# Kernel optimization log

Hardware: AMD Instinct MI355X
Metric: run time of the kernel (lower is better)

The kernel has to match this reference:

```python
import jax, jax.numpy as jnp
import numpy as np

B, T, D = 8, 2048, 1024
H, C, DV = 8, 64, 128   # n_heads, latent_dim, d_head
LN_EPS = 1e-5
NORM_EPS = 1e-12  # F.normalize eps


def _xavier(k, shape, fan_in, fan_out):
    lim = float(np.sqrt(6.0 / (fan_in + fan_out)))
    return jax.random.uniform(k, shape, jnp.float32, -lim, lim)


def setup_inputs() -> dict:
    key = jax.random.key(0)
    ks = jax.random.split(key, 9)
    x = jax.random.normal(ks[0], (B, T, D), jnp.float32)
    Wq = _xavier(ks[1], (C, D), D, C)            # S_q weight (out,in)
    Wk = _xavier(ks[2], (C, D), D, C)            # S_k
    Wv = _xavier(ks[3], (C, D), D, C)            # S_v
    Qc = _xavier(ks[4], (H, C, C), C, C)         # per-head latent rotations
    Vc = _xavier(ks[5], (H, C, DV), C, DV)       # per-head value up-proj
    Wa_w = _xavier(ks[6], (H * C, D), D, H * C)  # W_alpha weight
    Wa_b = jnp.full((H * C,), 3.0, jnp.float32)  # W_alpha bias init = 3.0
    Wo = _xavier(ks[7], (D, H * DV), H * DV, D)  # output proj
    gamma = jnp.ones((D,), jnp.float32)
    beta = jnp.zeros((D,), jnp.float32)
    return {"x": x, "Wq": Wq, "Wk": Wk, "Wv": Wv, "Qc": Qc, "Vc": Vc,
            "Wa_w": Wa_w, "Wa_b": Wa_b, "Wo": Wo, "gamma": gamma, "beta": beta}


def _forward(x, Wq, Wk, Wv, Qc, Vc, Wa_w, Wa_b, Wo, gamma, beta):
    residual = x
    # LayerNorm (biased variance, like torch)
    mu = jnp.mean(x, axis=-1, keepdims=True)
    var = jnp.mean(jnp.square(x - mu), axis=-1, keepdims=True)
    xn = (x - mu) * jax.lax.rsqrt(var + LN_EPS) * gamma + beta

    q_lat = xn @ Wq.T          # (B,T,C)
    k_lat = xn @ Wk.T          # (B,T,C) shared across heads
    v_lat = xn @ Wv.T          # (B,T,C)

    q = jnp.einsum('btc,hce->bhte', q_lat, Qc)   # (B,H,T,C)
    v = jnp.einsum('btc,hcd->bhtd', v_lat, Vc)   # (B,H,T,DV)
    alpha = jax.nn.sigmoid(xn @ Wa_w.T + Wa_b)   # (B,T,H*C)
    alpha = alpha.reshape(x.shape[0], x.shape[1], H, C).transpose(0, 2, 1, 3)  # (B,H,T,C)

    # F.normalize(k, dim=-1): k / max(||k||, eps)
    kn = k_lat / jnp.maximum(jnp.linalg.norm(k_lat, axis=-1, keepdims=True), NORM_EPS)

    # time-major for scan
    qs = jnp.moveaxis(q, 2, 0)      # (T,B,H,C)
    vs = jnp.moveaxis(v, 2, 0)      # (T,B,H,DV)
    als = jnp.moveaxis(alpha, 2, 0)  # (T,B,H,C)
    kns = jnp.moveaxis(kn, 1, 0)    # (T,B,C)

    S0 = jnp.zeros((x.shape[0], H, C, DV), x.dtype)

    def step(S, inp):
        q_t, k_t, v_t, a_t = inp
        # S_t = diag(alpha_t) S_{t-1} + k_t v_t^T  (k shared across heads)
        S = a_t[..., None] * S + k_t[:, None, :, None] * v_t[..., None, :]
        o_t = jnp.einsum('bhcv,bhc->bhv', S, q_t)
        return S, o_t

    _, outs = jax.lax.scan(step, S0, (qs, kns, vs, als))  # outs: (T,B,H,DV)
    out = jnp.moveaxis(outs, 0, 1).reshape(x.shape[0], x.shape[1], H * DV)
    return out @ Wo.T + residual


def reference(x, Wq, Wk, Wv, Qc, Vc, Wa_w, Wa_b, Wo, gamma, beta):
    return _forward(x, Wq, Wk, Wv, Qc, Vc, Wa_w, Wa_b, Wo, gamma, beta)
```

## Files before the change

kernel.cpp:

```cpp
#include <hip/hip_runtime.h>

typedef unsigned short u16;
typedef unsigned int   u32;
typedef __bf16 bf16x8 __attribute__((ext_vector_type(8)));
typedef float  f32x4  __attribute__((ext_vector_type(4)));

#define B_  8
#define T_  2048
#define D_  1024
#define H_  8
#define C_  64
#define DV_ 128
#define M_  (B_*T_)
#define L_  128
#define NC_ (T_/L_)
#define TS_ 8

__device__ __forceinline__ u16 f2bf(float f){
  u32 u = __float_as_uint(f);
  u32 r = (u + 0x7fffu + ((u >> 16) & 1u)) >> 16;
  return (u16)r;
}
__device__ __forceinline__ float bf2f(u16 u){
  return __uint_as_float(((u32)u) << 16);
}

__global__ __launch_bounds__(256) void ln_kernel(
    const float* __restrict__ x, const float* __restrict__ gamma,
    const float* __restrict__ beta, u16* __restrict__ xnb){
  const int m = blockIdx.x;
  const int tid = threadIdx.x;
  const int wave = tid >> 6, lane = tid & 63;
  const float* xr = x + (size_t)m * D_;
  float4 xv = *(const float4*)&xr[tid*4];
  float s = xv.x + xv.y + xv.z + xv.w;
  #pragma unroll
  for (int off = 32; off > 0; off >>= 1) s += __shfl_xor(s, off, 64);
  __shared__ float red[8];
  if (lane == 0) red[wave] = s;
  __syncthreads();
  float mu = (red[0]+red[1]+red[2]+red[3]) * (1.f/1024.f);
  float dx = xv.x-mu, dy = xv.y-mu, dz = xv.z-mu, dw = xv.w-mu;
  float ss = dx*dx + dy*dy + dz*dz + dw*dw;
  #pragma unroll
  for (int off = 32; off > 0; off >>= 1) ss += __shfl_xor(ss, off, 64);
  if (lane == 0) red[4+wave] = ss;
  __syncthreads();
  float var = (red[4]+red[5]+red[6]+red[7]) * (1.f/1024.f);
  float rs = rsqrtf(var + 1e-5f);
  float4 g  = *(const float4*)&gamma[tid*4];
  float4 bb = *(const float4*)&beta[tid*4];
  ushort4 o4;
  o4.x = f2bf(dx*rs*g.x + bb.x);
  o4.y = f2bf(dy*rs*g.y + bb.y);
  o4.z = f2bf(dz*rs*g.z + bb.z);
  o4.w = f2bf(dw*rs*g.w + bb.w);
  *(ushort4*)&xnb[(size_t)m*D_ + tid*4] = o4;
}

__global__ __launch_bounds__(256) void prep_weights(
    const float* __restrict__ Wq, const float* __restrict__ Wk,
    const float* __restrict__ Wv, const float* __restrict__ Wa,
    const float* __restrict__ Qc, const float* __restrict__ Vc,
    const float* __restrict__ Wo,
    u16* __restrict__ Wcatb, u16* __restrict__ QcTb,
    u16* __restrict__ VcTb,  u16* __restrict__ Wob){
  int idx = blockIdx.x * 256 + threadIdx.x;
  if (idx < 720896){
    int r = idx >> 10, col = idx & 1023;
    float v;
    if (r < 64)       v = Wq[(size_t)r*1024 + col];
    else if (r < 128) v = Wk[(size_t)(r-64)*1024 + col];
    else if (r < 192) v = Wv[(size_t)(r-128)*1024 + col];
    else              v = Wa[(size_t)(r-192)*1024 + col];
    Wcatb[idx] = f2bf(v);
  } else if (idx < 753664){
    int i = idx - 720896;
    int n = i >> 6, c = i & 63; int h = n >> 6, e = n & 63;
    QcTb[i] = f2bf(Qc[((size_t)h*64 + c)*64 + e]);
  } else if (idx < 819200){
    int i = idx - 753664;
    int n = i >> 6, c = i & 63; int h = n >> 7, d = n & 127;
    VcTb[i] = f2bf(Vc[((size_t)h*64 + c)*128 + d]);
  } else if (idx < 1867776){
    int i = idx - 819200;
    Wob[i] = f2bf(Wo[i]);
  }
}

__global__ __launch_bounds__(256) void gemm_bf16(
    const u16* __restrict__ A, const u16* __restrict__ Bw,
    float* __restrict__ C, const float* __restrict__ res,
    u16* __restrict__ Cb, int N, int K){
  __shared__ u16 As[128][36];
  __shared__ u16 Bs[64][36];
  const int tid = threadIdx.x;
  const int wave = tid >> 6;
  const int lane = tid & 63;
  const int q  = lane >> 4;
  const int mr = lane & 15;
  const int m0 = blockIdx.x * 128;
  const int n0 = blockIdx.y * 64;

  union FragU { u32 u[4]; bf16x8 v; };
  f32x4 zero = {0.f, 0.f, 0.f, 0.f};
  f32x4 acc[2][4];
  #pragma unroll
  for (int i = 0; i < 2; i++)
    #pragma unroll
    for (int j = 0; j < 4; j++) acc[i][j] = zero;

  for (int k0 = 0; k0 < K; k0 += 32){
    #pragma unroll
    for (int p = 0; p < 2; ++p){
      int ch = p*256 + tid;
      int r = ch >> 2, c4 = ch & 3;
      const uint4 val = *(const uint4*)(&A[(size_t)(m0 + r)*K + k0 + c4*8]);
      u32* dst = (u32*)&As[r][c4*8];
      dst[0]=val.x; dst[1]=val.y; dst[2]=val.z; dst[3]=val.w;
    }
    {
      int r = tid >> 2, c4 = tid & 3;
      const uint4 val = *(const uint4*)(&Bw[(size_t)(n0 + r)*K + k0 + c4*8]);
      u32* dst = (u32*)&Bs[r][c4*8];
      dst[0]=val.x; dst[1]=val.y; dst[2]=val.z; dst[3]=val.w;
    }
    __syncthreads();
    bf16x8 afr[2], bfr[4];
    #pragma unroll
    for (int mt = 0; mt < 2; mt++){
      const u32* p = (const u32*)&As[wave*32 + mt*16 + mr][q*8];
      FragU f; f.u[0]=p[0]; f.u[1]=p[1]; f.u[2]=p[2]; f.u[3]=p[3];
      afr[mt] = f.v;
    }
    #pragma unroll
    for (int nt = 0; nt < 4; nt++){
      const u32* p = (const u32*)&Bs[nt*16 + mr][q*8];
      FragU f; f.u[0]=p[0]; f.u[1]=p[1]; f.u[2]=p[2]; f.u[3]=p[3];
      bfr[nt] = f.v;
    }
    #pragma unroll
    for (int mt = 0; mt < 2; mt++)
      #pragma unroll
      for (int nt = 0; nt < 4; nt++)
        acc[mt][nt] = __builtin_amdgcn_mfma_f32_16x16x32_bf16(
            afr[mt], bfr[nt], acc[mt][nt], 0, 0, 0);
    __syncthreads();
  }

  #pragma unroll
  for (int mt = 0; mt < 2; mt++)
    #pragma unroll
    for (int nt = 0; nt < 4; nt++)
      #pragma unroll
      for (int r = 0; r < 4; r++){
        int row = m0 + wave*32 + mt*16 + q*4 + r;
        int col = n0 + nt*16 + mr;
        size_t idx = (size_t)row * N + col;
        float v = acc[mt][nt][r];
        if (res) v += res[idx];
        if (Cb) Cb[idx] = f2bf(v);
        else    C[idx] = v;
      }
}

__global__ __launch_bounds__(256) void split_proj(
    const float* __restrict__ proj, const float* __restrict__ Wab,
    u16* __restrict__ qlatb, float* __restrict__ knf,
    u16* __restrict__ vlatb, float* __restrict__ alphaf){
  const int m = blockIdx.x * 4 + (threadIdx.x >> 6);
  const int lane = threadIdx.x & 63;
  const float* pr = proj + (size_t)m * 704;
  qlatb[(size_t)m*64 + lane] = f2bf(pr[lane]);
  float kv = pr[64 + lane];
  float ss = kv * kv;
  #pragma unroll
  for (int off = 32; off > 0; off >>= 1) ss += __shfl_xor(ss, off, 64);
  float nrm = fmaxf(sqrtf(ss), 1e-12f);
  knf[(size_t)m*64 + lane] = kv / nrm;
  vlatb[(size_t)m*64 + lane] = f2bf(pr[128 + lane]);
  #pragma unroll
  for (int j = 0; j < 8; j++){
    int jj = j*64 + lane;
    float av = pr[192 + jj] + Wab[jj];
    alphaf[(size_t)m*512 + jj] = 1.f / (1.f + expf(-av));
  }
}


__global__ __launch_bounds__(512, 2) void scan_pass1(
    const float* __restrict__ knf, const u16* __restrict__ vb,
    const float* __restrict__ alphaf,
    float* __restrict__ Sbuf, float* __restrict__ btot){
  const int ch = blockIdx.x;
  const int bh = blockIdx.y;
  const int b = bh >> 3, h = bh & 7;
  const int tid = threadIdx.x;
  const int g = tid >> 7;
  const int d = tid & 127;
  const int t0 = ch * L_;
  __shared__ __align__(16) float sK[TS_][64];
  __shared__ __align__(16) float sA[TS_][64];
  __shared__ __align__(16) float sV[TS_][128];

  const float* kbase = knf    + ((size_t)(b*T_ + t0))*64;
  const float* abase = alphaf + ((size_t)(b*T_ + t0))*512 + h*64;
  const u16*   vbase = vb     + ((size_t)(b*T_ + t0))*1024 + h*128;

  float S[16];
  #pragma unroll
  for (int i = 0; i < 16; i++) S[i] = 0.f;
  float bt = 1.f;

  const int ts = tid >> 6, cs = tid & 63;
  for (int sb = 0; sb < L_/TS_; sb++){
    const int tb = sb * TS_;
    sK[ts][cs] = kbase[(size_t)(tb+ts)*64 + cs];
    sA[ts][cs] = abase[(size_t)(tb+ts)*512 + cs];
    {
      int i1 = 512 + tid;
      sV[tid>>7][tid&127] = bf2f(vbase[(size_t)(tb+(tid>>7))*1024 + (tid&127)]);
      sV[i1 >>7][i1 &127] = bf2f(vbase[(size_t)(tb+(i1 >>7))*1024 + (i1 &127)]);
    }
    __syncthreads();
    #pragma unroll 1
    for (int tt = 0; tt < TS_; tt++){
      const float vd = sV[tt][d];
      #pragma unroll
      for (int i4 = 0; i4 < 4; i4++){
        float4 a4 = *(const float4*)&sA[tt][g*16 + i4*4];
        float4 k4 = *(const float4*)&sK[tt][g*16 + i4*4];
        S[i4*4+0] = a4.x*S[i4*4+0] + k4.x*vd;
        S[i4*4+1] = a4.y*S[i4*4+1] + k4.y*vd;
        S[i4*4+2] = a4.z*S[i4*4+2] + k4.z*vd;
        S[i4*4+3] = a4.w*S[i4*4+3] + k4.w*vd;
      }
      if (d < 16) bt *= sA[tt][g*16 + d];
      __builtin_amdgcn_sched_barrier(0);
    }
    __syncthreads();
  }
  float* Sl = Sbuf + ((size_t)bh*NC_ + ch) * (64*128);
  #pragma unroll
  for (int i = 0; i < 16; i++) Sl[(size_t)(g*16+i)*128 + d] = S[i];
  if (d < 16) btot[((size_t)bh*NC_ + ch)*64 + g*16 + d] = bt;
}

__global__ __launch_bounds__(256) void scan_combine(
    float* __restrict__ Sbuf, const float* __restrict__ btot){
  const int bh = blockIdx.x;
  const int tid = threadIdx.x;
  float S[32];
  #pragma unroll
  for (int i = 0; i < 32; i++) S[i] = 0.f;
  float*       Sb  = Sbuf + (size_t)bh*NC_*8192;
  const float* btb = btot + (size_t)bh*NC_*64;
  for (int j = 0; j < NC_; j++){
    if (j < NC_-1){
      #pragma unroll
      for (int i = 0; i < 32; i++){
        int e = i*256 + tid;
        float loc = Sb[(size_t)j*8192 + e];
        float bv  = btb[j*64 + (e >> 7)];
        Sb[(size_t)j*8192 + e] = S[i];
        S[i] = bv * S[i] + loc;
      }
    } else {
      #pragma unroll
      for (int i = 0; i < 32; i++) Sb[(size_t)j*8192 + i*256 + tid] = S[i];
    }
  }
}

__global__ __launch_bounds__(512, 2) void scan_pass2(
    const float* __restrict__ qf, const float* __restrict__ knf,
    const u16* __restrict__ vb, const float* __restrict__ alphaf,
    const float* __restrict__ Sbuf, u16* __restrict__ ob){
  const int ch = blockIdx.x;
  const int bh = blockIdx.y;
  const int b = bh >> 3, h = bh & 7;
  const int tid = threadIdx.x;
  const int g = tid >> 7;
  const int d = tid & 127;
  const int t0 = ch * L_;
  __shared__ __align__(16) float sQ[TS_][64];
  __shared__ __align__(16) float sK[TS_][64];
  __shared__ __align__(16) float sA[TS_][64];
  __shared__ __align__(16) float sV[TS_][128];
  __shared__ __align__(16) float sO[4][TS_][128];

  const float* qbase = qf     + ((size_t)(b*T_ + t0))*512 + h*64;
  const float* kbase = knf    + ((size_t)(b*T_ + t0))*64;
  const float* abase = alphaf + ((size_t)(b*T_ + t0))*512 + h*64;
  const u16*   vbase = vb     + ((size_t)(b*T_ + t0))*1024 + h*128;
  u16*         obase = ob     + ((size_t)(b*T_ + t0))*1024 + h*128;

  float S[16];
  const float* Si = Sbuf + ((size_t)bh*NC_ + ch) * (64*128);
  #pragma unroll
  for (int i = 0; i < 16; i++) S[i] = Si[(size_t)(g*16+i)*128 + d];

  const int ts = tid >> 6, cs = tid & 63;
  for (int sb = 0; sb < L_/TS_; sb++){
    const int tb = sb * TS_;
    sQ[ts][cs] = qbase[(size_t)(tb+ts)*512 + cs];
    sK[ts][cs] = kbase[(size_t)(tb+ts)*64 + cs];
    sA[ts][cs] = abase[(size_t)(tb+ts)*512 + cs];
    {
      int i1 = 512 + tid;
      sV[tid>>7][tid&127] = bf2f(vbase[(size_t)(tb+(tid>>7))*1024 + (tid&127)]);
      sV[i1 >>7][i1 &127] = bf2f(vbase[(size_t)(tb+(i1 >>7))*1024 + (i1 &127)]);
    }
    __syncthreads();
    #pragma unroll 1
    for (int tt = 0; tt < TS_; tt++){
      const float vd = sV[tt][d];
      float o = 0.f;
      #pragma unroll
      for (int i4 = 0; i4 < 4; i4++){
        float4 a4 = *(const float4*)&sA[tt][g*16 + i4*4];
        float4 k4 = *(const float4*)&sK[tt][g*16 + i4*4];
        float4 q4 = *(const float4*)&sQ[tt][g*16 + i4*4];
        S[i4*4+0] = a4.x*S[i4*4+0] + k4.x*vd;  o += S[i4*4+0]*q4.x;
        S[i4*4+1] = a4.y*S[i4*4+1] + k4.y*vd;  o += S[i4*4+1]*q4.y;
        S[i4*4+2] = a4.z*S[i4*4+2] + k4.z*vd;  o += S[i4*4+2]*q4.z;
        S[i4*4+3] = a4.w*S[i4*4+3] + k4.w*vd;  o += S[i4*4+3]*q4.w;
      }
      sO[g][tt][d] = o;
      __builtin_amdgcn_sched_barrier(0);
    }
    __syncthreads();
    #pragma unroll
    for (int i = 0; i < 2; i++){
      int idx = i*512 + tid;
      int tt = idx >> 7, dd = idx & 127;
      float o = sO[0][tt][dd] + sO[1][tt][dd] + sO[2][tt][dd] + sO[3][tt][dd];
      obase[(size_t)(tb+tt)*1024 + dd] = f2bf(o);
    }
  }
}

extern "C" void kernel_launch(void* const* d_in, const int* in_sizes, int n_in,
                              void* d_out, int out_size, void* d_ws, size_t ws_size,
                              hipStream_t stream){
  const float* x     = (const float*)d_in[0];
  const float* Wq    = (const float*)d_in[1];
  const float* Wk    = (const float*)d_in[2];
  const float* Wv    = (const float*)d_in[3];
  const float* Qc    = (const float*)d_in[4];
  const float* Vc    = (const float*)d_in[5];
  const float* Wa_w  = (const float*)d_in[6];
  const float* Wa_b  = (const float*)d_in[7];
  const float* Wo    = (const float*)d_in[8];
  const float* gamma = (const float*)d_in[9];
  const float* beta  = (const float*)d_in[10];
  float* out = (float*)d_out;

  char* ws = (char*)d_ws;
  size_t off = 0;
  auto alloc = [&](size_t bytes) -> void* {
    void* p = ws + off; off += (bytes + 255) & ~(size_t)255; return p;
  };
  char* R1 = (char*)alloc((size_t)M_ * 1024 * 2);
  u16*   xnb  = (u16*)R1;
  u16*   obuf = (u16*)R1;
  char* R2 = (char*)alloc((size_t)M_ * 704 * 4);
  float* proj = (float*)R2;
  float* qf   = (float*)R2;
  float* Sbuf   = (float*)alloc((size_t)64 * NC_ * 8192 * 4);
  u16*   vfb    = (u16*)alloc((size_t)M_ * 1024 * 2);
  float* alphaf = (float*)alloc((size_t)M_ * 512 * 4);
  float* knf    = (float*)alloc((size_t)M_ * 64 * 4);
  u16*   qlatb  = (u16*)alloc((size_t)M_ * 64 * 2);
  u16*   vlatb  = (u16*)alloc((size_t)M_ * 64 * 2);
  u16*   Wcatb  = (u16*)alloc((size_t)704 * 1024 * 2);
  u16*   QcTb   = (u16*)alloc((size_t)512 * 64 * 2);
  u16*   VcTb   = (u16*)alloc((size_t)1024 * 64 * 2);
  u16*   Wob    = (u16*)alloc((size_t)1024 * 1024 * 2);
  float* btotp  = (float*)alloc((size_t)64 * NC_ * 64 * 4);
  (void)ws_size; (void)in_sizes; (void)n_in; (void)out_size;

  ln_kernel<<<dim3(M_), dim3(256), 0, stream>>>(x, gamma, beta, xnb);
  prep_weights<<<dim3(7296), dim3(256), 0, stream>>>(
      Wq, Wk, Wv, Wa_w, Qc, Vc, Wo, Wcatb, QcTb, VcTb, Wob);
  gemm_bf16<<<dim3(M_/128, 704/64), dim3(256), 0, stream>>>(
      xnb, Wcatb, proj, nullptr, nullptr, 704, 1024);
  split_proj<<<dim3(M_/4), dim3(256), 0, stream>>>(
      proj, Wa_b, qlatb, knf, vlatb, alphaf);
  gemm_bf16<<<dim3(M_/128, 1024/64), dim3(256), 0, stream>>>(
      vlatb, VcTb, nullptr, nullptr, vfb, 1024, 64);
  gemm_bf16<<<dim3(M_/128, 512/64), dim3(256), 0, stream>>>(
      qlatb, QcTb, qf, nullptr, nullptr, 512, 64);
  scan_pass1<<<dim3(NC_-1, 64), dim3(512), 0, stream>>>(
      knf, vfb, alphaf, Sbuf, btotp);
  scan_combine<<<dim3(64), dim3(256), 0, stream>>>(Sbuf, btotp);
  scan_pass2<<<dim3(NC_, 64), dim3(512), 0, stream>>>(
      qf, knf, vfb, alphaf, Sbuf, obuf);
  gemm_bf16<<<dim3(M_/128, 1024/64), dim3(256), 0, stream>>>(
      obuf, Wob, out, x, nullptr, 1024, 1024);
}
```

Before: 567.7 us.

## Load scan k/alpha/q via scalar loads instead of LDS staging in scan passes

Both scan kernels stop staging k, alpha, q and v through shared memory with block barriers. Each wave now reads its 16-element alpha/k/q slices straight into scalar registers with inline s_load_dwordx16, and reads v directly from global memory. Launch bounds are raised so more blocks can be resident per CU. This targets LDS traffic and barrier stalls, but each timestep now waits on a scalar-load round trip. The added barrier in pass2 guards reuse of the sO buffer across sub-blocks.

```diff
diff --git a/kernel.cpp b/kernel.cpp
--- a/kernel.cpp
+++ b/kernel.cpp
@@ -4,6 +4,7 @@
 typedef unsigned int   u32;
 typedef __bf16 bf16x8 __attribute__((ext_vector_type(8)));
 typedef float  f32x4  __attribute__((ext_vector_type(4)));
+typedef float  f32x16 __attribute__((ext_vector_type(16)));
 
 #define B_  8
 #define T_  2048
@@ -188,7 +189,26 @@
 }
 
 
-__global__ __launch_bounds__(512, 2) void scan_pass1(
+__device__ __forceinline__ void sload2(const float* ap, const float* kp,
+                                       f32x16& a16, f32x16& k16){
+  asm volatile("s_load_dwordx16 %0, %2, 0x0\n\t"
+               "s_load_dwordx16 %1, %3, 0x0\n\t"
+               "s_waitcnt lgkmcnt(0)"
+               : "=&s"(a16), "=&s"(k16)
+               : "s"(ap), "s"(kp));
+}
+__device__ __forceinline__ void sload3(const float* ap, const float* kp,
+                                       const float* qp,
+                                       f32x16& a16, f32x16& k16, f32x16& q16){
+  asm volatile("s_load_dwordx16 %0, %3, 0x0\n\t"
+               "s_load_dwordx16 %1, %4, 0x0\n\t"
+               "s_load_dwordx16 %2, %5, 0x0\n\t"
+               "s_waitcnt lgkmcnt(0)"
+               : "=&s"(a16), "=&s"(k16), "=&s"(q16)
+               : "s"(ap), "s"(kp), "s"(qp));
+}
+
+__global__ __launch_bounds__(512, 8) void scan_pass1(
     const float* __restrict__ knf, const u16* __restrict__ vb,
     const float* __restrict__ alphaf,
     float* __restrict__ Sbuf, float* __restrict__ btot){
@@ -196,50 +216,32 @@
   const int bh = blockIdx.y;
   const int b = bh >> 3, h = bh & 7;
   const int tid = threadIdx.x;
-  const int g = tid >> 7;
+  const int g = __builtin_amdgcn_readfirstlane(tid >> 7);
   const int d = tid & 127;
   const int t0 = ch * L_;
-  __shared__ __align__(16) float sK[TS_][64];
-  __shared__ __align__(16) float sA[TS_][64];
-  __shared__ __align__(16) float sV[TS_][128];
-
-  const float* kbase = knf    + ((size_t)(b*T_ + t0))*64;
-  const float* abase = alphaf + ((size_t)(b*T_ + t0))*512 + h*64;
-  const u16*   vbase = vb     + ((size_t)(b*T_ + t0))*1024 + h*128;
+
+  const float* kp = knf    + ((size_t)(b*T_ + t0))*64  + g*16;
+  const float* ap = alphaf + ((size_t)(b*T_ + t0))*512 + h*64 + g*16;
+  const u16*   vp = vb     + ((size_t)(b*T_ + t0))*1024 + h*128 + d;
 
   float S[16];
   #pragma unroll
   for (int i = 0; i < 16; i++) S[i] = 0.f;
   float bt = 1.f;
 
-  const int ts = tid >> 6, cs = tid & 63;
-  for (int sb = 0; sb < L_/TS_; sb++){
-    const int tb = sb * TS_;
-    sK[ts][cs] = kbase[(size_t)(tb+ts)*64 + cs];
-    sA[ts][cs] = abase[(size_t)(tb+ts)*512 + cs];
-    {
-      int i1 = 512 + tid;
-      sV[tid>>7][tid&127] = bf2f(vbase[(size_t)(tb+(tid>>7))*1024 + (tid&127)]);
-      sV[i1 >>7][i1 &127] = bf2f(vbase[(size_t)(tb+(i1 >>7))*1024 + (i1 &127)]);
-    }
-    __syncthreads();
-    #pragma unroll 1
-    for (int tt = 0; tt < TS_; tt++){
-      const float vd = sV[tt][d];
-      #pragma unroll
-      for (int i4 = 0; i4 < 4; i4++){
-        float4 a4 = *(const float4*)&sA[tt][g*16 + i4*4];
-        float4 k4 = *(const float4*)&sK[tt][g*16 + i4*4];
-        S[i4*4+0] = a4.x*S[i4*4+0] + k4.x*vd;
-        S[i4*4+1] = a4.y*S[i4*4+1] + k4.y*vd;
-        S[i4*4+2] = a4.z*S[i4*4+2] + k4.z*vd;
-        S[i4*4+3] = a4.w*S[i4*4+3] + k4.w*vd;
-      }
-      if (d < 16) bt *= sA[tt][g*16 + d];
-      __builtin_amdgcn_sched_barrier(0);
-    }
-    __syncthreads();
-  }
+  for (int t = 0; t < L_; t++){
+    float vd = bf2f(vp[0]);
+    float al = 1.f;
+    if (d < 16) al = ap[d];
+    f32x16 a16, k16;
+    sload2(ap, kp, a16, k16);
+    #pragma unroll
+    for (int i = 0; i < 16; i++)
+      S[i] = a16[i]*S[i] + k16[i]*vd;
+    bt *= al;
+    kp += 64; ap += 512; vp += 1024;
+  }
+
   float* Sl = Sbuf + ((size_t)bh*NC_ + ch) * (64*128);
   #pragma unroll
   for (int i = 0; i < 16; i++) Sl[(size_t)(g*16+i)*128 + d] = S[i];
@@ -272,7 +274,7 @@
   }
 }
 
-__global__ __launch_bounds__(512, 2) void scan_pass2(
+__global__ __launch_bounds__(512, 8) void scan_pass2(
     const float* __restrict__ qf, const float* __restrict__ knf,
     const u16* __restrict__ vb, const float* __restrict__ alphaf,
     const float* __restrict__ Sbuf, u16* __restrict__ ob){
@@ -280,54 +282,38 @@
   const int bh = blockIdx.y;
   const int b = bh >> 3, h = bh & 7;
   const int tid = threadIdx.x;
-  const int g = tid >> 7;
+  const int g = __builtin_amdgcn_readfirstlane(tid >> 7);
   const int d = tid & 127;
   const int t0 = ch * L_;
-  __shared__ __align__(16) float sQ[TS_][64];
-  __shared__ __align__(16) float sK[TS_][64];
-  __shared__ __align__(16) float sA[TS_][64];
-  __shared__ __align__(16) float sV[TS_][128];
   __shared__ __align__(16) float sO[4][TS_][128];
 
-  const float* qbase = qf     + ((size_t)(b*T_ + t0))*512 + h*64;
-  const float* kbase = knf    + ((size_t)(b*T_ + t0))*64;
-  const float* abase = alphaf + ((size_t)(b*T_ + t0))*512 + h*64;
-  const u16*   vbase = vb     + ((size_t)(b*T_ + t0))*1024 + h*128;
-  u16*         obase = ob     + ((size_t)(b*T_ + t0))*1024 + h*128;
+  const float* qp = qf     + ((size_t)(b*T_ + t0))*512 + h*64 + g*16;
+  const float* kp = knf    + ((size_t)(b*T_ + t0))*64  + g*16;
+  const float* ap = alphaf + ((size_t)(b*T_ + t0))*512 + h*64 + g*16;
+  const u16*   vp = vb     + ((size_t)(b*T_ + t0))*1024 + h*128 + d;
+  u16*         obase = ob  + ((size_t)(b*T_ + t0))*1024 + h*128;
 
   float S[16];
   const float* Si = Sbuf + ((size_t)bh*NC_ + ch) * (64*128);
   #pragma unroll
   for (int i = 0; i < 16; i++) S[i] = Si[(size_t)(g*16+i)*128 + d];
 
-  const int ts = tid >> 6, cs = tid & 63;
   for (int sb = 0; sb < L_/TS_; sb++){
-    const int tb = sb * TS_;
-    sQ[ts][cs] = qbase[(size_t)(tb+ts)*512 + cs];
-    sK[ts][cs] = kbase[(size_t)(tb+ts)*64 + cs];
-    sA[ts][cs] = abase[(size_t)(tb+ts)*512 + cs];
-    {
-      int i1 = 512 + tid;
-      sV[tid>>7][tid&127] = bf2f(vbase[(size_t)(tb+(tid>>7))*1024 + (tid&127)]);
-      sV[i1 >>7][i1 &127] = bf2f(vbase[(size_t)(tb+(i1 >>7))*1024 + (i1 &127)]);
-    }
-    __syncthreads();
-    #pragma unroll 1
+    #pragma unroll
     for (int tt = 0; tt < TS_; tt++){
-      const float vd = sV[tt][d];
-      float o = 0.f;
-      #pragma unroll
-      for (int i4 = 0; i4 < 4; i4++){
-        float4 a4 = *(const float4*)&sA[tt][g*16 + i4*4];
-        float4 k4 = *(const float4*)&sK[tt][g*16 + i4*4];
-        float4 q4 = *(const float4*)&sQ[tt][g*16 + i4*4];
-        S[i4*4+0] = a4.x*S[i4*4+0] + k4.x*vd;  o += S[i4*4+0]*q4.x;
-        S[i4*4+1] = a4.y*S[i4*4+1] + k4.y*vd;  o += S[i4*4+1]*q4.y;
-        S[i4*4+2] = a4.z*S[i4*4+2] + k4.z*vd;  o += S[i4*4+2]*q4.z;
-        S[i4*4+3] = a4.w*S[i4*4+3] + k4.w*vd;  o += S[i4*4+3]*q4.w;
+      float vd = bf2f(vp[0]);
+      f32x16 a16, k16, q16;
+      sload3(ap, kp, qp, a16, k16, q16);
+      float o0 = 0.f, o1 = 0.f, o2 = 0.f, o3 = 0.f;
+      #pragma unroll
+      for (int i = 0; i < 16; i += 4){
+        S[i+0] = a16[i+0]*S[i+0] + k16[i+0]*vd;  o0 += S[i+0]*q16[i+0];
+        S[i+1] = a16[i+1]*S[i+1] + k16[i+1]*vd;  o1 += S[i+1]*q16[i+1];
+        S[i+2] = a16[i+2]*S[i+2] + k16[i+2]*vd;  o2 += S[i+2]*q16[i+2];
+        S[i+3] = a16[i+3]*S[i+3] + k16[i+3]*vd;  o3 += S[i+3]*q16[i+3];
       }
-      sO[g][tt][d] = o;
-      __builtin_amdgcn_sched_barrier(0);
+      sO[g][tt][d] = (o0+o1)+(o2+o3);
+      kp += 64; ap += 512; qp += 512; vp += 1024;
     }
     __syncthreads();
     #pragma unroll
@@ -335,8 +321,9 @@
       int idx = i*512 + tid;
       int tt = idx >> 7, dd = idx & 127;
       float o = sO[0][tt][dd] + sO[1][tt][dd] + sO[2][tt][dd] + sO[3][tt][dd];
-      obase[(size_t)(tb+tt)*1024 + dd] = f2bf(o);
-    }
+      obase[(size_t)(sb*TS_+tt)*1024 + dd] = f2bf(o);
+    }
+    __syncthreads();
   }
 }
 
```

New measurement: 544.5 us. -4.1%, faster.
